# Kernel tuning notes

Measured on AMD Instinct MI355X. Metric: run time of the kernel, lower is better.

The kernel has to match this reference:

```python
import jax, jax.numpy as jnp
import numpy as np

D_MODEL = 1024
NUM_HEADS = 16
HEAD_DIM = D_MODEL // NUM_HEADS  # 64
MAX_SEQ_LEN = 2048
BASE = 10000.0


def _rope_tables(seq_len):
    # theta_i = base^(-2i/hd) for i in [0, hd/2)
    theta = 1.0 / (BASE ** (jnp.arange(0, HEAD_DIM, 2, dtype=jnp.float32) / HEAD_DIM))
    angles = jnp.arange(seq_len, dtype=jnp.float32)[:, None] * theta  # [S, hd/2]
    return jnp.cos(angles), jnp.sin(angles)


def _apply_rope(x, cos, sin):
    # x: [B, H, S, hd]; cos/sin: [S, hd/2] broadcast over B,H
    x1 = x[..., 0::2]
    x2 = x[..., 1::2]
    r1 = x1 * cos - x2 * sin
    r2 = x1 * sin + x2 * cos
    return jnp.stack([r1, r2], axis=-1).reshape(x.shape)  # interleave back


def setup_inputs() -> dict:
    key = jax.random.key(0)
    k_x, k_q, k_k, k_v, k_o = jax.random.split(key, 5)
    B, S = 2, 2048
    x = jax.random.normal(k_x, (B, S, D_MODEL), dtype=jnp.float32)
    init = 0.02
    w_q = jax.random.normal(k_q, (D_MODEL, D_MODEL), dtype=jnp.float32) * init
    w_k = jax.random.normal(k_k, (D_MODEL, D_MODEL), dtype=jnp.float32) * init
    w_v = jax.random.normal(k_v, (D_MODEL, D_MODEL), dtype=jnp.float32) * init
    w_o = jax.random.normal(k_o, (D_MODEL, D_MODEL), dtype=jnp.float32) * init
    return {"x": x, "w_q": w_q, "w_k": w_k, "w_v": w_v, "w_o": w_o}


def reference(x, w_q, w_k, w_v, w_o):
    # Prefill path: start_pos=0, cache=None, eval-mode dropout (identity).
    B, S, D = x.shape
    H, hd = NUM_HEADS, HEAD_DIM
    scale = 1.0 / (hd ** 0.5)

    # nn.Linear(bias=False): y = x @ W.T
    q = (x @ w_q.T).reshape(B, S, H, hd).transpose(0, 2, 1, 3)  # [B,H,S,hd]
    k = (x @ w_k.T).reshape(B, S, H, hd).transpose(0, 2, 1, 3)
    v = (x @ w_v.T).reshape(B, S, H, hd).transpose(0, 2, 1, 3)

    cos, sin = _rope_tables(S)  # same tables for every head (per-head torch loop vectorized)
    q_rot = _apply_rope(q, cos, sin)
    k_rot = _apply_rope(k, cos, sin)

    attn = jnp.einsum("bhqd,bhkd->bhqk", q_rot, k_rot) * scale  # [B,H,S,S]
    # causal mask: triu(ones(S,S), diagonal = S_k - S_q + 1 = 1)
    causal = jnp.triu(jnp.ones((S, S), dtype=bool), k=1)
    attn = jnp.where(causal[None, None], -jnp.inf, attn)
    attn_w = jax.nn.softmax(attn, axis=-1)

    out = jnp.einsum("bhqk,bhkd->bhqd", attn_w, v)  # [B,H,S,hd]
    out = out.transpose(0, 2, 1, 3).reshape(B, S, D)
    return out @ w_o.T
```

## Files before the change

kernel.cpp:

```cpp
#include <hip/hip_runtime.h>
#include <hip/hip_bf16.h>
#include <math.h>


#define S_LEN 2048
#define NHEADS 16
#define HD 64
#define DM 1024

typedef __attribute__((ext_vector_type(8))) short bf16x8;
typedef __attribute__((ext_vector_type(4))) float f32x4;

#define MFMA16(a, b, c) __builtin_amdgcn_mfma_f32_16x16x32_bf16((a), (b), (c), 0, 0, 0)
#define NEG_BIG (-1e30f)

#if __has_builtin(__builtin_amdgcn_exp2f)
#define EXP2F(x) __builtin_amdgcn_exp2f(x)
#else
#define EXP2F(x) exp2f(x)
#endif

#define GLOAD_LDS16(g, l)                                                      \
    __builtin_amdgcn_global_load_lds(                                          \
        (const __attribute__((address_space(1))) void*)(g),                    \
        (__attribute__((address_space(3))) void*)(l), 16, 0, 0)

__global__ __launch_bounds__(256) void convert_kernel(
    const float* __restrict__ x,  const float* __restrict__ wq,
    const float* __restrict__ wk, const float* __restrict__ wv,
    const float* __restrict__ wo,
    __hip_bfloat16* __restrict__ xb,  __hip_bfloat16* __restrict__ wqb,
    __hip_bfloat16* __restrict__ wkb, __hip_bfloat16* __restrict__ wvb,
    __hip_bfloat16* __restrict__ wob, float2* __restrict__ tab)
{
    const int y = blockIdx.y;
    if (y == 8) {
        const int gid = blockIdx.x * 256 + threadIdx.x;
        if (gid < S_LEN * 32) {
            const int s = gid >> 5, p = gid & 31;
            float theta = powf(10000.0f, -(float)(2 * p) * (1.0f / 64.0f));
            float sn, cs;
            sincosf((float)s * theta, &sn, &cs);
            tab[gid] = make_float2(cs, sn);
        }
        return;
    }
    const float* src;
    __hip_bfloat16* dst;
    size_t off = 0;
    if (y < 4)      { src = x;  dst = xb;  off = (size_t)y * 1048576; }
    else if (y == 4) { src = wq; dst = wqb; }
    else if (y == 5) { src = wk; dst = wkb; }
    else if (y == 6) { src = wv; dst = wvb; }
    else             { src = wo; dst = wob; }

    const size_t i = off + ((size_t)blockIdx.x * 256 + threadIdx.x) * 4;
    float4 v = *(const float4*)(src + i);
    __hip_bfloat16 t[4] = { __float2bfloat16(v.x), __float2bfloat16(v.y),
                            __float2bfloat16(v.z), __float2bfloat16(v.w) };
    *(ushort4*)(dst + i) = *(ushort4*)t;
}

__global__ __launch_bounds__(256) void qkv_kernel(
    const __hip_bfloat16* __restrict__ X,
    const __hip_bfloat16* __restrict__ Wq,
    const __hip_bfloat16* __restrict__ Wk,
    const __hip_bfloat16* __restrict__ Wv,
    __hip_bfloat16* __restrict__ qws,
    __hip_bfloat16* __restrict__ kws,
    __hip_bfloat16* __restrict__ vws)
{
    const int z = blockIdx.z;
    const bool vz = (z == 2);
    const __hip_bfloat16* __restrict__ Asrc = vz ? Wv : X;
    const __hip_bfloat16* __restrict__ Bsrc = vz ? X : ((z == 0) ? Wq : Wk);
    __hip_bfloat16* __restrict__ out = (z == 0) ? qws : (z == 1) ? kws : vws;

    __shared__ __align__(16) __hip_bfloat16 Asm[128 * 32];
    __shared__ __align__(16) __hip_bfloat16 Bsm[128 * 32];

    const int tid = threadIdx.x;
    const int wave = tid >> 6, lane = tid & 63;
    const int quad = lane >> 4, l15 = lane & 15;
    const int wm = (wave >> 1) * 64, wn = (wave & 1) * 64;
    const int m0 = vz ? blockIdx.x * 128 : blockIdx.y * 128;
    const int n0 = vz ? blockIdx.y * 128 : blockIdx.x * 128;

    f32x4 acc[4][4] = {};

    for (int k0 = 0; k0 < DM; k0 += 32) {
#pragma unroll
        for (int c = 0; c < 2; c++) {
            int idx = c * 2048 + tid * 8;
            int r = idx >> 5, kc = idx & 31;
            GLOAD_LDS16(Asrc + (size_t)(m0 + r) * DM + k0 + kc, &Asm[idx]);
            GLOAD_LDS16(Bsrc + (size_t)(n0 + r) * DM + k0 + kc, &Bsm[idx]);
        }
        __syncthreads();
        bf16x8 af[4], bfv[4];
#pragma unroll
        for (int i = 0; i < 4; i++)
            af[i] = *(const bf16x8*)(&Asm[(wm + i * 16 + l15) * 32 + quad * 8]);
#pragma unroll
        for (int j = 0; j < 4; j++)
            bfv[j] = *(const bf16x8*)(&Bsm[(wn + j * 16 + l15) * 32 + quad * 8]);
#pragma unroll
        for (int i = 0; i < 4; i++)
#pragma unroll
            for (int j = 0; j < 4; j++)
                acc[i][j] = MFMA16(af[i], bfv[j], acc[i][j]);
        __syncthreads();
    }

#pragma unroll
    for (int i = 0; i < 4; i++) {
#pragma unroll
        for (int r = 0; r < 4; r++) {
            int m = m0 + wm + i * 16 + quad * 4 + r;
#pragma unroll
            for (int j = 0; j < 4; j++) {
                int col = n0 + wn + j * 16 + l15;
                size_t idx;
                if (vz) {
                    int h = m >> 6, d = m & 63;
                    int b = col >> 11, s = col & 2047;
                    idx = (((size_t)(b * NHEADS + h)) * HD + d) * S_LEN + s;
                } else {
                    int b = m >> 11, s = m & 2047;
                    int h = col >> 6, d = col & 63;
                    idx = (((size_t)(b * NHEADS + h)) * S_LEN + s) * HD + d;
                }
                out[idx] = __float2bfloat16(acc[i][j][r]);
            }
        }
    }
}

__global__ __launch_bounds__(256) void rope_kernel(
    __hip_bfloat16* __restrict__ q, __hip_bfloat16* __restrict__ k,
    const float2* __restrict__ tab)
{
    __hip_bfloat16* __restrict__ p = (blockIdx.y == 0) ? q : k;
    const float qscale = (blockIdx.y == 0) ? 0.18033688011112042f
                                           : 1.0f;
    const int gid = blockIdx.x * 256 + threadIdx.x;
    const int e0 = gid * 8;
    const int s = (gid >> 3) & 2047;
    const int p4 = (gid & 7) * 4;

    const float2* tp = tab + s * 32 + p4;
    float4 t01 = *(const float4*)(tp);
    float4 t23 = *(const float4*)(tp + 2);
    float cs[4] = { t01.x, t01.z, t23.x, t23.z };
    float sn[4] = { t01.y, t01.w, t23.y, t23.w };

    int4 raw = *(const int4*)(p + e0);
    __hip_bfloat16* v = (__hip_bfloat16*)&raw;
#pragma unroll
    for (int i = 0; i < 4; i++) {
        float x1 = __bfloat162float(v[2 * i]);
        float x2 = __bfloat162float(v[2 * i + 1]);
        v[2 * i]     = __float2bfloat16((x1 * cs[i] - x2 * sn[i]) * qscale);
        v[2 * i + 1] = __float2bfloat16((x1 * sn[i] + x2 * cs[i]) * qscale);
    }
    *(int4*)(p + e0) = raw;
}


#define SMPV(sc, mm, ll, oo, Pr)                                               \
    do {                                                                       \
        float pm[4];                                                           \
        _Pragma("unroll")                                                      \
        for (int r = 0; r < 4; r++)                                            \
            pm[r] = fmaxf(fmaxf(sc[0][r], sc[1][r]),                           \
                          fmaxf(sc[2][r], sc[3][r]));                          \
        bool ok = true;                                                        \
        _Pragma("unroll")                                                      \
        for (int r = 0; r < 4; r++) ok = ok && (pm[r] <= mm[r] + 11.0f);       \
        if (!__all(ok)) {                                                      \
            _Pragma("unroll")                                                  \
            for (int off = 1; off < 16; off <<= 1)                             \
                _Pragma("unroll")                                              \
                for (int r = 0; r < 4; r++)                                    \
                    pm[r] = fmaxf(pm[r], __shfl_xor(pm[r], off));              \
            _Pragma("unroll")                                                  \
            for (int r = 0; r < 4; r++) {                                      \
                float mn = fmaxf(mm[r], pm[r]);                                \
                float al = EXP2F(mm[r] - mn);                                  \
                mm[r] = mn;                                                    \
                ll[r] *= al;                                                   \
                _Pragma("unroll")                                              \
                for (int t = 0; t < 4; t++) oo[t][r] *= al;                    \
            }                                                                  \
        }                                                                      \
        _Pragma("unroll")                                                      \
        for (int t = 0; t < 4; t++)                                            \
            _Pragma("unroll")                                                  \
            for (int r = 0; r < 4; r++)                                        \
                Pr[(quad * 4 + r) * 72 + t * 16 + l15] =                       \
                    __float2bfloat16(EXP2F(sc[t][r] - mm[r]));                 \
        _Pragma("unroll")                                                      \
        for (int st = 0; st < 2; st++) {                                       \
            bf16x8 pf = *(const bf16x8*)(&Pr[l15 * 72 + st * 32 + quad * 8]);  \
            __builtin_amdgcn_s_setprio(1);                                     \
            ll = MFMA16(pf, ones, ll);                                         \
            _Pragma("unroll")                                                  \
            for (int t = 0; t < 4; t++) oo[t] = MFMA16(pf, vf[st][t], oo[t]);  \
            __builtin_amdgcn_s_setprio(0);                                     \
        }                                                                      \
    } while (0)

#define LOAD_VF(kv0)                                                           \
    do {                                                                       \
        _Pragma("unroll")                                                      \
        for (int st = 0; st < 2; st++)                                         \
            _Pragma("unroll")                                                  \
            for (int t = 0; t < 4; t++)                                        \
                vf[st][t] = *(const bf16x8*)(Vtb +                             \
                    (size_t)(t * 16 + l15) * S_LEN + (kv0) + st * 32 + quad * 8); \
    } while (0)

#define LOAD_KF(kv0)                                                           \
    do {                                                                       \
        _Pragma("unroll")                                                      \
        for (int st = 0; st < 2; st++)                                         \
            _Pragma("unroll")                                                  \
            for (int t = 0; t < 4; t++)                                        \
                kf[st][t] = *(const bf16x8*)(Kb +                              \
                    (size_t)((kv0) + t * 16 + l15) * HD + st * 32 + quad * 8); \
    } while (0)

#define QK(sc, qf)                                                             \
    do {                                                                       \
        __builtin_amdgcn_s_setprio(1);                                         \
        _Pragma("unroll")                                                      \
        for (int st = 0; st < 2; st++)                                         \
            _Pragma("unroll")                                                  \
            for (int t = 0; t < 4; t++) sc[t] = MFMA16(qf[st], kf[st][t], sc[t]); \
        __builtin_amdgcn_s_setprio(0);                                         \
    } while (0)

#define MASK(sc, rowbase, kv0)                                                 \
    do {                                                                       \
        _Pragma("unroll")                                                      \
        for (int t = 0; t < 4; t++) {                                          \
            int col = (kv0) + t * 16 + l15;                                    \
            _Pragma("unroll")                                                  \
            for (int r = 0; r < 4; r++) {                                      \
                int row = (rowbase) + quad * 4 + r;                            \
                if (col > row) sc[t][r] = NEG_BIG;                             \
            }                                                                  \
        }                                                                      \
    } while (0)

__global__ __launch_bounds__(256) void attn_kernel(
    const __hip_bfloat16* __restrict__ Qg,
    const __hip_bfloat16* __restrict__ Kg,
    const __hip_bfloat16* __restrict__ Vtg,
    __hip_bfloat16* __restrict__ Og)
{
    const int bh = blockIdx.x;
    const int qi = (blockIdx.y < 8) ? blockIdx.y : 23 - blockIdx.y;
    const int tid = threadIdx.x;
    const int w = tid >> 6, lane = tid & 63;
    const int quad = lane >> 4, l15 = lane & 15;
    const size_t base = (size_t)bh * S_LEN * HD;
    const __hip_bfloat16* Qb = Qg + base;
    const __hip_bfloat16* Kb = Kg + base;
    const __hip_bfloat16* Vtb = Vtg + base;
    const int b = bh >> 4, h = bh & 15;

    __shared__ __align__(16) __hip_bfloat16 Pl[128 * 72];
    __hip_bfloat16* PrA = &Pl[w * 32 * 72];
    __hip_bfloat16* PrB = PrA + 16 * 72;

    const int q0 = qi * 128;
    const int rowA = q0 + w * 16;
    const int rowB = rowA + 64;

    bf16x8 qfA[2], qfB[2];
#pragma unroll
    for (int st = 0; st < 2; st++) {
        qfA[st] = *(const bf16x8*)(Qb + (size_t)(rowA + l15) * HD + st * 32 + quad * 8);
        qfB[st] = *(const bf16x8*)(Qb + (size_t)(rowB + l15) * HD + st * 32 + quad * 8);
    }

    bf16x8 ones;
#pragma unroll
    for (int i = 0; i < 8; i++) ones[i] = (short)0x3F80;

    float mA[4], mB[4];
    f32x4 lA = {}, lB = {};
    f32x4 oA[4] = {}, oB[4] = {};
#pragma unroll
    for (int r = 0; r < 4; r++) { mA[r] = NEG_BIG; mB[r] = NEG_BIG; }

    bf16x8 kf[2][4];
    bf16x8 vf[2][4];
    LOAD_KF(0);

#pragma unroll 1
    for (int j = 0; j < 2 * qi; j++) {
        const int kv0 = j * 64;
        LOAD_VF(kv0);
        f32x4 scA[4] = {}, scB[4] = {};
        QK(scA, qfA);
        QK(scB, qfB);
        LOAD_KF(kv0 + 64);
        SMPV(scA, mA, lA, oA, PrA);
        SMPV(scB, mB, lB, oB, PrB);
    }

    {
        const int kv0 = q0;
        LOAD_VF(kv0);
        f32x4 scA[4] = {}, scB[4] = {};
        QK(scA, qfA);
        QK(scB, qfB);
        LOAD_KF(kv0 + 64);
        MASK(scA, rowA, kv0);
        SMPV(scA, mA, lA, oA, PrA);
        SMPV(scB, mB, lB, oB, PrB);
    }

    {
        const int kv0 = q0 + 64;
        LOAD_VF(kv0);
        f32x4 scB[4] = {};
        QK(scB, qfB);
        MASK(scB, rowB, kv0);
        SMPV(scB, mB, lB, oB, PrB);
    }

#pragma unroll
    for (int t = 0; t < 4; t++)
#pragma unroll
        for (int r = 0; r < 4; r++) {
            int d = t * 16 + l15;
            int sA = rowA + quad * 4 + r;
            Og[((size_t)(b * S_LEN + sA)) * DM + h * HD + d] =
                __float2bfloat16(oA[t][r] / lA[r]);
            int sB = rowB + quad * 4 + r;
            Og[((size_t)(b * S_LEN + sB)) * DM + h * HD + d] =
                __float2bfloat16(oB[t][r] / lB[r]);
        }
}

__global__ __launch_bounds__(256) void oproj_kernel(
    const __hip_bfloat16* __restrict__ A,
    const __hip_bfloat16* __restrict__ W,
    float* __restrict__ out)
{
    __shared__ __align__(16) __hip_bfloat16 Asm[128 * 32];
    __shared__ __align__(16) __hip_bfloat16 Bsm[128 * 32];

    const int tid = threadIdx.x;
    const int wave = tid >> 6, lane = tid & 63;
    const int quad = lane >> 4, l15 = lane & 15;
    const int wm = (wave >> 1) * 64, wn = (wave & 1) * 64;
    const int m0 = blockIdx.y * 128, n0 = blockIdx.x * 128;

    f32x4 acc[4][4] = {};

    for (int k0 = 0; k0 < DM; k0 += 32) {
#pragma unroll
        for (int c = 0; c < 2; c++) {
            int idx = c * 2048 + tid * 8;
            int r = idx >> 5, kc = idx & 31;
            GLOAD_LDS16(A + (size_t)(m0 + r) * DM + k0 + kc, &Asm[idx]);
            GLOAD_LDS16(W + (size_t)(n0 + r) * DM + k0 + kc, &Bsm[idx]);
        }
        __syncthreads();
        bf16x8 af[4], bfv[4];
#pragma unroll
        for (int i = 0; i < 4; i++)
            af[i] = *(const bf16x8*)(&Asm[(wm + i * 16 + l15) * 32 + quad * 8]);
#pragma unroll
        for (int j = 0; j < 4; j++)
            bfv[j] = *(const bf16x8*)(&Bsm[(wn + j * 16 + l15) * 32 + quad * 8]);
#pragma unroll
        for (int i = 0; i < 4; i++)
#pragma unroll
            for (int j = 0; j < 4; j++)
                acc[i][j] = MFMA16(af[i], bfv[j], acc[i][j]);
        __syncthreads();
    }

#pragma unroll
    for (int i = 0; i < 4; i++)
#pragma unroll
        for (int r = 0; r < 4; r++) {
            int m = m0 + wm + i * 16 + quad * 4 + r;
#pragma unroll
            for (int j = 0; j < 4; j++) {
                int col = n0 + wn + j * 16 + l15;
                __hip_bfloat16 bb = __float2bfloat16(acc[i][j][r]);
                unsigned int u = ((unsigned int)(*(unsigned short*)&bb)) << 16;
                out[(size_t)m * DM + col] = __uint_as_float(u);
            }
        }
}

extern "C" void kernel_launch(void* const* d_in, const int* in_sizes, int n_in,
                              void* d_out, int out_size, void* d_ws, size_t ws_size,
                              hipStream_t stream)
{
    const float* x  = (const float*)d_in[0];
    const float* wq = (const float*)d_in[1];
    const float* wk = (const float*)d_in[2];
    const float* wv = (const float*)d_in[3];
    const float* wo = (const float*)d_in[4];
    float* out = (float*)d_out;

    const size_t xe = (size_t)2 * S_LEN * DM;
    const size_t we = (size_t)DM * DM;
    __hip_bfloat16* xb  = (__hip_bfloat16*)d_ws;
    __hip_bfloat16* wqb = xb + xe;
    __hip_bfloat16* wkb = wqb + we;
    __hip_bfloat16* wvb = wkb + we;
    __hip_bfloat16* wob = wvb + we;
    __hip_bfloat16* qws = wob + we;
    __hip_bfloat16* kws = qws + xe;
    __hip_bfloat16* vws = kws + xe;
    __hip_bfloat16* aws = vws + xe;
    float2* tab = (float2*)aws;

    dim3 blk(256, 1, 1);
    convert_kernel<<<dim3(1024, 9, 1), blk, 0, stream>>>(x, wq, wk, wv, wo,
                                                         xb, wqb, wkb, wvb, wob, tab);
    qkv_kernel<<<dim3(8, 32, 3), blk, 0, stream>>>(xb, wqb, wkb, wvb, qws, kws, vws);
    rope_kernel<<<dim3(2048, 2, 1), blk, 0, stream>>>(qws, kws, tab);
    attn_kernel<<<dim3(32, 16, 1), blk, 0, stream>>>(qws, kws, vws, aws);
    oproj_kernel<<<dim3(8, 32, 1), blk, 0, stream>>>(aws, wob, out);
}
```

Before: 209.6 us.

## Split attention into one-wave blocks per 16-row query tile, longest first

Attention now launches one 64-thread block per 16 query rows, giving 4096 blocks instead of 512 blocks of four waves. Blocks are ordered so the longest causal rows are scheduled first. Each wave handles a single row tile, which frees registers and shared memory and should smooth load balance across CUs. In exchange, each wave loads K/V fragments from global memory independently, with no reuse across waves or across the A/B row pair, so K/V traffic rises and per-block launch overhead increases.

```diff
diff --git a/kernel.cpp b/kernel.cpp
--- a/kernel.cpp
+++ b/kernel.cpp
@@ -253,16 +253,15 @@
         }                                                                      \
     } while (0)
 
-__global__ __launch_bounds__(256) void attn_kernel(
+__global__ __launch_bounds__(64) void attn_kernel(
     const __hip_bfloat16* __restrict__ Qg,
     const __hip_bfloat16* __restrict__ Kg,
     const __hip_bfloat16* __restrict__ Vtg,
     __hip_bfloat16* __restrict__ Og)
 {
     const int bh = blockIdx.x;
-    const int qi = (blockIdx.y < 8) ? blockIdx.y : 23 - blockIdx.y;
-    const int tid = threadIdx.x;
-    const int w = tid >> 6, lane = tid & 63;
+    const int a = 127 - blockIdx.y;
+    const int lane = threadIdx.x & 63;
     const int quad = lane >> 4, l15 = lane & 15;
     const size_t base = (size_t)bh * S_LEN * HD;
     const __hip_bfloat16* Qb = Qg + base;
@@ -270,66 +269,47 @@
     const __hip_bfloat16* Vtb = Vtg + base;
     const int b = bh >> 4, h = bh & 15;
 
-    __shared__ __align__(16) __hip_bfloat16 Pl[128 * 72];
-    __hip_bfloat16* PrA = &Pl[w * 32 * 72];
-    __hip_bfloat16* PrB = PrA + 16 * 72;
-
-    const int q0 = qi * 128;
-    const int rowA = q0 + w * 16;
-    const int rowB = rowA + 64;
-
-    bf16x8 qfA[2], qfB[2];
-#pragma unroll
-    for (int st = 0; st < 2; st++) {
-        qfA[st] = *(const bf16x8*)(Qb + (size_t)(rowA + l15) * HD + st * 32 + quad * 8);
-        qfB[st] = *(const bf16x8*)(Qb + (size_t)(rowB + l15) * HD + st * 32 + quad * 8);
-    }
+    __shared__ __align__(16) __hip_bfloat16 Prow[16 * 72];
+
+    const int rowA = a * 16;
+    const int jD = a >> 2;
+
+    bf16x8 qf[2];
+#pragma unroll
+    for (int st = 0; st < 2; st++)
+        qf[st] = *(const bf16x8*)(Qb + (size_t)(rowA + l15) * HD + st * 32 + quad * 8);
 
     bf16x8 ones;
 #pragma unroll
     for (int i = 0; i < 8; i++) ones[i] = (short)0x3F80;
 
-    float mA[4], mB[4];
-    f32x4 lA = {}, lB = {};
-    f32x4 oA[4] = {}, oB[4] = {};
-#pragma unroll
-    for (int r = 0; r < 4; r++) { mA[r] = NEG_BIG; mB[r] = NEG_BIG; }
+    float mA[4];
+    f32x4 lA = {};
+    f32x4 oA[4] = {};
+#pragma unroll
+    for (int r = 0; r < 4; r++) mA[r] = NEG_BIG;
 
     bf16x8 kf[2][4];
     bf16x8 vf[2][4];
     LOAD_KF(0);
 
 #pragma unroll 1
-    for (int j = 0; j < 2 * qi; j++) {
+    for (int j = 0; j < jD; j++) {
         const int kv0 = j * 64;
         LOAD_VF(kv0);
-        f32x4 scA[4] = {}, scB[4] = {};
-        QK(scA, qfA);
-        QK(scB, qfB);
+        f32x4 sc[4] = {};
+        QK(sc, qf);
         LOAD_KF(kv0 + 64);
-        SMPV(scA, mA, lA, oA, PrA);
-        SMPV(scB, mB, lB, oB, PrB);
+        SMPV(sc, mA, lA, oA, Prow);
     }
 
     {
-        const int kv0 = q0;
+        const int kv0 = jD * 64;
         LOAD_VF(kv0);
-        f32x4 scA[4] = {}, scB[4] = {};
-        QK(scA, qfA);
-        QK(scB, qfB);
-        LOAD_KF(kv0 + 64);
-        MASK(scA, rowA, kv0);
-        SMPV(scA, mA, lA, oA, PrA);
-        SMPV(scB, mB, lB, oB, PrB);
-    }
-
-    {
-        const int kv0 = q0 + 64;
-        LOAD_VF(kv0);
-        f32x4 scB[4] = {};
-        QK(scB, qfB);
-        MASK(scB, rowB, kv0);
-        SMPV(scB, mB, lB, oB, PrB);
+        f32x4 sc[4] = {};
+        QK(sc, qf);
+        MASK(sc, rowA, kv0);
+        SMPV(sc, mA, lA, oA, Prow);
     }
 
 #pragma unroll
@@ -340,9 +320,6 @@
             int sA = rowA + quad * 4 + r;
             Og[((size_t)(b * S_LEN + sA)) * DM + h * HD + d] =
                 __float2bfloat16(oA[t][r] / lA[r]);
-            int sB = rowB + quad * 4 + r;
-            Og[((size_t)(b * S_LEN + sB)) * DM + h * HD + d] =
-                __float2bfloat16(oB[t][r] / lB[r]);
         }
 }
 
@@ -430,6 +407,6 @@
                                                          xb, wqb, wkb, wvb, wob, tab);
     qkv_kernel<<<dim3(8, 32, 3), blk, 0, stream>>>(xb, wqb, wkb, wvb, qws, kws, vws);
     rope_kernel<<<dim3(2048, 2, 1), blk, 0, stream>>>(qws, kws, tab);
-    attn_kernel<<<dim3(32, 16, 1), blk, 0, stream>>>(qws, kws, vws, aws);
+    attn_kernel<<<dim3(32, 128, 1), dim3(64, 1, 1), 0, stream>>>(qws, kws, vws, aws);
     oproj_kernel<<<dim3(8, 32, 1), blk, 0, stream>>>(aws, wob, out);
 }
```

After: 270.5 us. +29.1%, slower.

## Software-pipeline QK of next KV tile ahead of softmax and PV

Applied to the files above, without the earlier changes.

Splits the combined softmax+PV macro into a softmax/P-store stage and a PV accumulate stage. The main loop now computes QK scores for the next KV tile before running softmax and PV on the current one, with a prologue and a reworked diagonal tail. The aim is to overlap the QK MFMA work with the exp/max work of softmax so the matrix units stay busy. In exchange each thread holds an extra set of score accumulators, which raises register pressure and may lower occupancy.

```diff
diff --git a/kernel.cpp b/kernel.cpp
--- a/kernel.cpp
+++ b/kernel.cpp
@@ -167,7 +167,7 @@
 }
 
 
-#define SMPV(sc, mm, ll, oo, Pr)                                               \
+#define SM_STORE(sc, mm, ll, oo, Pr)                                           \
     do {                                                                       \
         float pm[4];                                                           \
         _Pragma("unroll")                                                      \
@@ -199,6 +199,10 @@
             for (int r = 0; r < 4; r++)                                        \
                 Pr[(quad * 4 + r) * 72 + t * 16 + l15] =                       \
                     __float2bfloat16(EXP2F(sc[t][r] - mm[r]));                 \
+    } while (0)
+
+#define PV_ACC(ll, oo, Pr)                                                     \
+    do {                                                                       \
         _Pragma("unroll")                                                      \
         for (int st = 0; st < 2; st++) {                                       \
             bf16x8 pf = *(const bf16x8*)(&Pr[l15 * 72 + st * 32 + quad * 8]);  \
@@ -297,39 +301,45 @@
 
     bf16x8 kf[2][4];
     bf16x8 vf[2][4];
+
     LOAD_KF(0);
+    f32x4 scA[4] = {}, scB[4] = {};
+    QK(scA, qfA);
+    QK(scB, qfB);
+    LOAD_KF(64);
 
 #pragma unroll 1
     for (int j = 0; j < 2 * qi; j++) {
         const int kv0 = j * 64;
         LOAD_VF(kv0);
-        f32x4 scA[4] = {}, scB[4] = {};
-        QK(scA, qfA);
-        QK(scB, qfB);
-        LOAD_KF(kv0 + 64);
-        SMPV(scA, mA, lA, oA, PrA);
-        SMPV(scB, mB, lB, oB, PrB);
+        f32x4 scAn[4] = {}, scBn[4] = {};
+        QK(scAn, qfA);
+        QK(scBn, qfB);
+        LOAD_KF(kv0 + 128);
+        SM_STORE(scA, mA, lA, oA, PrA);
+        SM_STORE(scB, mB, lB, oB, PrB);
+        PV_ACC(lA, oA, PrA);
+        PV_ACC(lB, oB, PrB);
+#pragma unroll
+        for (int t = 0; t < 4; t++) { scA[t] = scAn[t]; scB[t] = scBn[t]; }
     }
 
     {
         const int kv0 = q0;
         LOAD_VF(kv0);
-        f32x4 scA[4] = {}, scB[4] = {};
-        QK(scA, qfA);
-        QK(scB, qfB);
-        LOAD_KF(kv0 + 64);
+        f32x4 scBn[4] = {};
+        QK(scBn, qfB);
         MASK(scA, rowA, kv0);
-        SMPV(scA, mA, lA, oA, PrA);
-        SMPV(scB, mB, lB, oB, PrB);
-    }
-
-    {
-        const int kv0 = q0 + 64;
-        LOAD_VF(kv0);
-        f32x4 scB[4] = {};
-        QK(scB, qfB);
-        MASK(scB, rowB, kv0);
-        SMPV(scB, mB, lB, oB, PrB);
+        SM_STORE(scA, mA, lA, oA, PrA);
+        SM_STORE(scB, mB, lB, oB, PrB);
+        PV_ACC(lA, oA, PrA);
+        PV_ACC(lB, oB, PrB);
+
+        const int kv1 = kv0 + 64;
+        LOAD_VF(kv1);
+        MASK(scBn, rowB, kv1);
+        SM_STORE(scBn, mB, lB, oB, PrB);
+        PV_ACC(lB, oB, PrB);
     }
 
 #pragma unroll
```

Measured after the change: 212.4 us. About the same (+1.4%).
